# Performance work log

Measured on AMD Instinct MI355X. Metric: run time of the kernel, lower is better.

## Reference

```python
import jax, jax.numpy as jnp
import numpy as np
from jax import lax

B, H_IMG, W_IMG = 512, 812, 40
HID = 128
NUM_CLASSES = 12
LSTM_IN = 32 * ((W_IMG - 5) // 2 + 1)  # 32 channels * 18 = 576


def setup_inputs() -> dict:
    key = jax.random.key(0)
    ks = jax.random.split(key, 20)
    s = 0.05
    inp = {
        "x": jax.random.normal(ks[0], (B, 1, H_IMG, W_IMG), jnp.float32),
        "conv_w": jax.random.normal(ks[1], (32, 1, 20, 5), jnp.float32) * s,
        "conv_b": jax.random.normal(ks[2], (32,), jnp.float32) * s,
        "Wih0": jax.random.normal(ks[3], (4 * HID, LSTM_IN), jnp.float32) * s,
        "Whh0": jax.random.normal(ks[4], (4 * HID, HID), jnp.float32) * s,
        "bih0": jax.random.normal(ks[5], (4 * HID,), jnp.float32) * s,
        "bhh0": jax.random.normal(ks[6], (4 * HID,), jnp.float32) * s,
        "Wih1": jax.random.normal(ks[7], (4 * HID, HID), jnp.float32) * s,
        "Whh1": jax.random.normal(ks[8], (4 * HID, HID), jnp.float32) * s,
        "bih1": jax.random.normal(ks[9], (4 * HID,), jnp.float32) * s,
        "bhh1": jax.random.normal(ks[10], (4 * HID,), jnp.float32) * s,
        "W_att": jax.random.normal(ks[11], (HID, HID), jnp.float32) * s,
        "b_att": jax.random.normal(ks[12], (HID,), jnp.float32) * s,
        "v_att": jax.random.normal(ks[13], (HID,), jnp.float32) * s,
        "W1": jax.random.normal(ks[14], (64, HID), jnp.float32) * s,
        "b1": jax.random.normal(ks[15], (64,), jnp.float32) * s,
        "W2": jax.random.normal(ks[16], (NUM_CLASSES, 64), jnp.float32) * s,
        "b2": jax.random.normal(ks[17], (NUM_CLASSES,), jnp.float32) * s,
    }
    return inp


def _lstm_layer(seq, Wih, Whh, bih, bhh):
    # seq: (T, B, I); PyTorch gate order i, f, g, o
    T, Bn, _ = seq.shape
    Hd = Whh.shape[1]
    x_proj = jnp.einsum('tbi,gi->tbg', seq, Wih) + bih + bhh  # (T,B,4H)

    def step(carry, xg):
        h, c = carry
        g = xg + h @ Whh.T
        i, f, gg, o = jnp.split(g, 4, axis=-1)
        c = jax.nn.sigmoid(f) * c + jax.nn.sigmoid(i) * jnp.tanh(gg)
        h = jax.nn.sigmoid(o) * jnp.tanh(c)
        return (h, c), h

    init = (jnp.zeros((Bn, Hd), seq.dtype), jnp.zeros((Bn, Hd), seq.dtype))
    _, hs = lax.scan(step, init, x_proj)
    return hs  # (T,B,H)


def _forward(x, conv_w, conv_b, Wih0, Whh0, bih0, bhh0, Wih1, Whh1, bih1, bhh1,
             W_att, b_att, v_att, W1, b1, W2, b2):
    # Conv2d(1->32, k=(20,5), s=(8,2)) + ReLU
    y = lax.conv_general_dilated(x, conv_w, (8, 2), 'VALID',
                                 dimension_numbers=('NCHW', 'OIHW', 'NCHW'))
    y = jax.nn.relu(y + conv_b[None, :, None, None])  # (B,32,T,W')
    b, c, t, w = y.shape
    # permute(0,2,3,1).view(b,t,-1).permute(1,0,2) -> (T,B,W'*32)
    seq = jnp.transpose(y, (2, 0, 3, 1)).reshape(t, b, w * c)
    # 2-layer LSTM (inter-layer dropout=0.2 inactive at eval)
    h1 = _lstm_layer(seq, Wih0, Whh0, bih0, bhh0)
    h2 = _lstm_layer(h1, Wih1, Whh1, bih1, bhh1)
    # additive attention pooling over time
    squish = jnp.tanh(jnp.einsum('tbh,hk->tbk', h2, W_att) + b_att)  # (T,B,H)
    attn = jnp.einsum('tbh,h->tb', squish, v_att)                     # (T,B)
    w_att_n = jax.nn.softmax(attn, axis=0)                            # softmax over T
    pooled = jnp.einsum('tb,tbh->bh', w_att_n, h2)                    # (B,H)
    # dnn1 -> (dropout inactive at eval) -> output
    hdn = pooled @ W1.T + b1
    return hdn @ W2.T + b2  # (B,num_classes)


def reference(x, conv_w, conv_b, Wih0, Whh0, bih0, bhh0, Wih1, Whh1, bih1, bhh1,
              W_att, b_att, v_att, W1, b1, W2, b2):
    return _forward(x, conv_w, conv_b, Wih0, Whh0, bih0, bhh0, Wih1, Whh1,
                    bih1, bhh1, W_att, b_att, v_att, W1, b1, W2, b2)
```

## Files before the change

### kernel.cpp

```cpp
#include <hip/hip_runtime.h>
#include <stdint.h>


#define T_STEPS 100
#define BATCH   512
#define HIDD    128
#define GATES   512
#define LSTMIN  576
#define HIMG    812
#define WIMG    40

typedef __attribute__((ext_vector_type(8))) short bf16x8;
typedef __attribute__((ext_vector_type(4))) float f32x4;

__device__ inline unsigned short f2bf(float f) {
  unsigned u = __float_as_uint(f);
  unsigned r = (u + 0x7fffu + ((u >> 16) & 1u)) >> 16;
  return (unsigned short)r;
}
__device__ inline float bf2f(unsigned short b) {
  return __uint_as_float(((unsigned)b) << 16);
}
__device__ inline float fsigm(float x) {
  float e = __expf(-x);
  return __builtin_amdgcn_rcpf(1.f + e);
}
__device__ inline float ftanh(float x) {
  float e = __expf(2.f * x);
  return (e - 1.f) * __builtin_amdgcn_rcpf(e + 1.f);
}
__device__ inline void lds_barrier() {
  asm volatile("s_waitcnt lgkmcnt(0)" ::: "memory");
  __builtin_amdgcn_s_barrier();
}

__global__ void prep_kernel(const float* __restrict__ Wih0, const float* __restrict__ Whh0,
                            const float* __restrict__ Wih1, const float* __restrict__ Whh1,
                            const float* __restrict__ Watt, const float* __restrict__ convw,
                            const float* __restrict__ bih0, const float* __restrict__ bhh0,
                            const float* __restrict__ bih1, const float* __restrict__ bhh1,
                            unsigned short* __restrict__ wih0b, unsigned short* __restrict__ whh0b,
                            unsigned short* __restrict__ wih1b, unsigned short* __restrict__ whh1b,
                            unsigned short* __restrict__ wattb, float* __restrict__ convwt,
                            float* __restrict__ bias0, float* __restrict__ bias1) {
  int tid = blockIdx.x * blockDim.x + threadIdx.x;
  int stride = gridDim.x * blockDim.x;
  for (int i = tid; i < GATES * LSTMIN; i += stride) wih0b[i] = f2bf(Wih0[i]);
  for (int i = tid; i < GATES * HIDD; i += stride) whh0b[i] = f2bf(Whh0[i]);
  for (int i = tid; i < GATES * HIDD; i += stride) wih1b[i] = f2bf(Wih1[i]);
  for (int i = tid; i < GATES * HIDD; i += stride) whh1b[i] = f2bf(Whh1[i]);
  for (int i = tid; i < HIDD * HIDD; i += stride) {
    int j = i >> 7, k = i & 127;
    wattb[i] = f2bf(Watt[k * HIDD + j]);
  }
  for (int i = tid; i < 3200; i += stride) {
    int k = i >> 5, c = i & 31;
    convwt[i] = convw[c * 100 + k];
  }
  for (int i = tid; i < GATES; i += stride) bias0[i] = bih0[i] + bhh0[i];
  for (int i = tid; i < GATES; i += stride) bias1[i] = bih1[i] + bhh1[i];
}

__global__ __launch_bounds__(256) void conv_kernel(const float* __restrict__ x,
                                                   const float* __restrict__ convwt,
                                                   const float* __restrict__ convb,
                                                   unsigned short* __restrict__ seq) {
  __shared__ __align__(16) float img[212 * WIMG];
  const int b = blockIdx.x;
  const int chunk = blockIdx.y;
  const int t0 = chunk * 25;
  const int row0 = 8 * t0;
  const float4* src = (const float4*)(x + (size_t)b * (HIMG * WIMG) + (size_t)row0 * WIMG);
  float4* dst = (float4*)img;
  for (int i = threadIdx.x; i < 212 * WIMG / 4; i += 256) dst[i] = src[i];
  __syncthreads();
  for (int p = threadIdx.x; p < 450; p += 256) {
    int tl = p / 18, wp = p % 18;
    int t = t0 + tl;
    float acc[32];
#pragma unroll
    for (int c = 0; c < 32; ++c) acc[c] = 0.f;
    const float* ibase = img + (8 * tl) * WIMG + 2 * wp;
#pragma unroll 2
    for (int kh = 0; kh < 20; ++kh) {
#pragma unroll
      for (int kw = 0; kw < 5; ++kw) {
        float iv = ibase[kh * WIMG + kw];
        const float* wk = convwt + (kh * 5 + kw) * 32;
#pragma unroll
        for (int c = 0; c < 32; ++c) acc[c] = fmaf(iv, wk[c], acc[c]);
      }
    }
    unsigned short* o = seq + ((size_t)(t * BATCH + b)) * LSTMIN + wp * 32;
#pragma unroll
    for (int c = 0; c < 32; ++c) {
      float v = acc[c] + convb[c];
      o[c] = f2bf(v > 0.f ? v : 0.f);
    }
  }
}

template <int KDIM>
__global__ __launch_bounds__(256) void gemm_xp_kernel(const unsigned short* __restrict__ A,
                                                      const unsigned short* __restrict__ Bw,
                                                      const float* __restrict__ bias,
                                                      unsigned short* __restrict__ Xp) {
  __shared__ __align__(16) unsigned short As[128 * 32];
  __shared__ __align__(16) unsigned short Bs[128 * 32];
  const int tid = threadIdx.x;
  const int lane = tid & 63;
  const int w = tid >> 6;
  const int col16 = lane & 15;
  const int q = lane >> 4;
  const int n0 = blockIdx.x * 128;
  const int m0 = blockIdx.y * 128;
  const int wm = (w & 1) * 64;
  const int wn = (w >> 1) * 64;
  f32x4 acc[4][4] = {};
  const int r = tid >> 2;
  const int sw = ((tid & 3) ^ (r & 3)) * 8;
  const unsigned wslot = (unsigned)w * 512;
  const unsigned short* ga = A + (size_t)(m0 + r) * KDIM + sw;
  const unsigned short* gb = Bw + (size_t)(n0 + r) * KDIM + sw;
  for (int k0 = 0; k0 < KDIM; k0 += 32) {
    __syncthreads();
    __builtin_amdgcn_global_load_lds((const __attribute__((address_space(1))) void*)(ga + k0),
                                     (__attribute__((address_space(3))) void*)(As + wslot), 16, 0, 0);
    __builtin_amdgcn_global_load_lds((const __attribute__((address_space(1))) void*)(ga + k0 + (size_t)64 * KDIM),
                                     (__attribute__((address_space(3))) void*)(As + wslot + 2048), 16, 0, 0);
    __builtin_amdgcn_global_load_lds((const __attribute__((address_space(1))) void*)(gb + k0),
                                     (__attribute__((address_space(3))) void*)(Bs + wslot), 16, 0, 0);
    __builtin_amdgcn_global_load_lds((const __attribute__((address_space(1))) void*)(gb + k0 + (size_t)64 * KDIM),
                                     (__attribute__((address_space(3))) void*)(Bs + wslot + 2048), 16, 0, 0);
    __syncthreads();
    bf16x8 af[4], bv[4];
#pragma unroll
    for (int i = 0; i < 4; ++i) {
      int ra = wm + i * 16 + col16;
      af[i] = *(const bf16x8*)(As + ra * 32 + ((q ^ (ra & 3)) * 8));
      int rb2 = wn + i * 16 + col16;
      bv[i] = *(const bf16x8*)(Bs + rb2 * 32 + ((q ^ (rb2 & 3)) * 8));
    }
#pragma unroll
    for (int i = 0; i < 4; ++i)
#pragma unroll
      for (int j = 0; j < 4; ++j)
        acc[i][j] = __builtin_amdgcn_mfma_f32_16x16x32_bf16(af[i], bv[j], acc[i][j], 0, 0, 0);
  }
#pragma unroll
  for (int ct = 0; ct < 4; ++ct) {
    int n = n0 + wn + ct * 16 + col16;
    float bvv = bias[n];
    int wS = (n >> 4) & 7;
    int ntS = n >> 7;
    int c16S = n & 15;
#pragma unroll
    for (int rt = 0; rt < 4; ++rt) {
      int m = m0 + wm + rt * 16 + q * 4;
      int t = m >> 9;
      int bb = m & 511;
      int blk = bb >> 4;
      int r16 = bb & 15;
      ushort4 u;
      u.x = f2bf(acc[rt][ct][0] + bvv);
      u.y = f2bf(acc[rt][ct][1] + bvv);
      u.z = f2bf(acc[rt][ct][2] + bvv);
      u.w = f2bf(acc[rt][ct][3] + bvv);
      size_t tile = (((size_t)t * 32 + blk) * 8 + wS) * 4 + ntS;
      *(ushort4*)(Xp + tile * 256 + c16S * 16 + r16) = u;
    }
  }
}

__global__ __launch_bounds__(512, 2) void scan_kernel(const unsigned short* __restrict__ Xp,
                                                      const unsigned short* __restrict__ Whh,
                                                      unsigned short* __restrict__ hout) {
  __shared__ __align__(16) unsigned short hlds[16 * 136];
  const int tid = threadIdx.x;
  const int lane = tid & 63;
  const int w = tid >> 6;
  const int col16 = lane & 15;
  const int q = lane >> 4;
  const int rb = blockIdx.x * 16;
  const int blk = blockIdx.x;

  bf16x8 bfrag[4][4];
  const unsigned short* xpb[4];
#pragma unroll
  for (int nt = 0; nt < 4; ++nt) {
    int cn = nt * HIDD + w * 16 + col16;
#pragma unroll
    for (int ks = 0; ks < 4; ++ks)
      bfrag[nt][ks] = *(const bf16x8*)(Whh + (size_t)cn * HIDD + ks * 32 + q * 8);
    xpb[nt] = Xp + (((size_t)blk * 8 + w) * 4 + nt) * 256 + col16 * 16 + q * 4;
  }
  for (int i = tid; i < 16 * 136; i += 512) hlds[i] = 0;
  float cst[4] = {0.f, 0.f, 0.f, 0.f};
  uint2 xb[4][4];
#pragma unroll
  for (int nt = 0; nt < 4; ++nt) xb[0][nt] = *(const uint2*)(xpb[nt]);
#pragma unroll
  for (int nt = 0; nt < 4; ++nt) xb[1][nt] = *(const uint2*)(xpb[nt] + GATES * BATCH);
  __syncthreads();

  const int srow = tid >> 5;
  const int scol = (tid & 31) * 4;

#pragma unroll 4
  for (int t = 0; t < T_STEPS; ++t) {
    if (t + 2 < T_STEPS) {
      int s2 = (t + 2) & 3;
#pragma unroll
      for (int nt = 0; nt < 4; ++nt)
        xb[s2][nt] = *(const uint2*)(xpb[nt] + (size_t)(t + 2) * (GATES * BATCH));
    }
    bf16x8 af[4];
#pragma unroll
    for (int ks = 0; ks < 4; ++ks)
      af[ks] = *(const bf16x8*)(hlds + col16 * 136 + ks * 32 + q * 8);
    f32x4 acc[4];
    const int s = t & 3;
#pragma unroll
    for (int nt = 0; nt < 4; ++nt) {
      uint2 xv = xb[s][nt];
      acc[nt][0] = __uint_as_float(xv.x << 16);
      acc[nt][1] = __uint_as_float(xv.x & 0xffff0000u);
      acc[nt][2] = __uint_as_float(xv.y << 16);
      acc[nt][3] = __uint_as_float(xv.y & 0xffff0000u);
    }
#pragma unroll
    for (int ks = 0; ks < 4; ++ks)
#pragma unroll
      for (int nt = 0; nt < 4; ++nt)
        acc[nt] = __builtin_amdgcn_mfma_f32_16x16x32_bf16(af[ks], bfrag[nt][ks], acc[nt], 0, 0, 0);
    unsigned short hv[4];
#pragma unroll
    for (int rr = 0; rr < 4; ++rr) {
      float pi = acc[0][rr], pf = acc[1][rr];
      float pg = acc[2][rr], po = acc[3][rr];
      float cc = fsigm(pf) * cst[rr] + fsigm(pi) * ftanh(pg);
      cst[rr] = cc;
      hv[rr] = f2bf(fsigm(po) * ftanh(cc));
    }
    lds_barrier();
    {
      int hc = w * 16 + col16;
#pragma unroll
      for (int rr = 0; rr < 4; ++rr)
        hlds[(q * 4 + rr) * 136 + hc] = hv[rr];
    }
    lds_barrier();
    ushort4 hx = *(const ushort4*)(hlds + srow * 136 + scol);
    *(ushort4*)(hout + ((size_t)(t * BATCH) + rb + srow) * HIDD + scol) = hx;
  }
}

__global__ __launch_bounds__(256) void gemm_att_kernel(const unsigned short* __restrict__ A,
                                                       const unsigned short* __restrict__ Bw,
                                                       const float* __restrict__ b_att,
                                                       const float* __restrict__ v_att,
                                                       float* __restrict__ scores) {
  __shared__ __align__(16) unsigned short As[128 * 32];
  __shared__ __align__(16) unsigned short Bs[128 * 32];
  __shared__ float s_red[128];
  const int tid = threadIdx.x;
  const int lane = tid & 63;
  const int w = tid >> 6;
  const int col16 = lane & 15;
  const int q = lane >> 4;
  const int m0 = blockIdx.y * 128;
  const int wm = (w & 1) * 64;
  const int wn = (w >> 1) * 64;
  f32x4 acc[4][4] = {};
  const int r = tid >> 2;
  const int sw = ((tid & 3) ^ (r & 3)) * 8;
  const unsigned wslot = (unsigned)w * 512;
  const unsigned short* ga = A + (size_t)(m0 + r) * HIDD + sw;
  const unsigned short* gb = Bw + (size_t)r * HIDD + sw;
  for (int k0 = 0; k0 < HIDD; k0 += 32) {
    __syncthreads();
    __builtin_amdgcn_global_load_lds((const __attribute__((address_space(1))) void*)(ga + k0),
                                     (__attribute__((address_space(3))) void*)(As + wslot), 16, 0, 0);
    __builtin_amdgcn_global_load_lds((const __attribute__((address_space(1))) void*)(ga + k0 + (size_t)64 * HIDD),
                                     (__attribute__((address_space(3))) void*)(As + wslot + 2048), 16, 0, 0);
    __builtin_amdgcn_global_load_lds((const __attribute__((address_space(1))) void*)(gb + k0),
                                     (__attribute__((address_space(3))) void*)(Bs + wslot), 16, 0, 0);
    __builtin_amdgcn_global_load_lds((const __attribute__((address_space(1))) void*)(gb + k0 + (size_t)64 * HIDD),
                                     (__attribute__((address_space(3))) void*)(Bs + wslot + 2048), 16, 0, 0);
    __syncthreads();
    bf16x8 af[4], bv[4];
#pragma unroll
    for (int i = 0; i < 4; ++i) {
      int ra = wm + i * 16 + col16;
      af[i] = *(const bf16x8*)(As + ra * 32 + ((q ^ (ra & 3)) * 8));
      int rb2 = wn + i * 16 + col16;
      bv[i] = *(const bf16x8*)(Bs + rb2 * 32 + ((q ^ (rb2 & 3)) * 8));
    }
#pragma unroll
    for (int i = 0; i < 4; ++i)
#pragma unroll
      for (int j = 0; j < 4; ++j)
        acc[i][j] = __builtin_amdgcn_mfma_f32_16x16x32_bf16(af[i], bv[j], acc[i][j], 0, 0, 0);
  }
  if (tid < 128) s_red[tid] = 0.f;
  float rs[4][4];
#pragma unroll
  for (int rt = 0; rt < 4; ++rt)
#pragma unroll
    for (int rr = 0; rr < 4; ++rr) rs[rt][rr] = 0.f;
#pragma unroll
  for (int ct = 0; ct < 4; ++ct) {
    int n = wn + ct * 16 + col16;
    float bvv = b_att[n], vv = v_att[n];
#pragma unroll
    for (int rt = 0; rt < 4; ++rt)
#pragma unroll
      for (int rr = 0; rr < 4; ++rr) {
        float xv2 = acc[rt][ct][rr] + bvv;
        float e = __expf(2.f * xv2);
        rs[rt][rr] += vv * (e - 1.f) * __builtin_amdgcn_rcpf(e + 1.f);
      }
  }
#pragma unroll
  for (int off = 1; off < 16; off <<= 1)
#pragma unroll
    for (int rt = 0; rt < 4; ++rt)
#pragma unroll
      for (int rr = 0; rr < 4; ++rr) rs[rt][rr] += __shfl_xor(rs[rt][rr], off, 64);
  __syncthreads();
  if (col16 == 0) {
#pragma unroll
    for (int rt = 0; rt < 4; ++rt)
#pragma unroll
      for (int rr = 0; rr < 4; ++rr)
        atomicAdd(&s_red[wm + rt * 16 + q * 4 + rr], rs[rt][rr]);
  }
  __syncthreads();
  if (tid < 128) scores[m0 + tid] = s_red[tid];
}

__global__ __launch_bounds__(128) void final_kernel(const float* __restrict__ scores,
                                                    const unsigned short* __restrict__ h2,
                                                    const float* __restrict__ W1, const float* __restrict__ b1,
                                                    const float* __restrict__ W2, const float* __restrict__ b2,
                                                    float* __restrict__ out) {
  const int b = blockIdx.x;
  const int tid = threadIdx.x;
  __shared__ float wj[T_STEPS];
  __shared__ float red[128];
  __shared__ float pooled[128];
  __shared__ float hdn[64];
  float sv = (tid < T_STEPS) ? scores[tid * BATCH + b] : -1e30f;
  red[tid] = sv;
  __syncthreads();
#pragma unroll
  for (int off = 64; off > 0; off >>= 1) {
    if (tid < off) red[tid] = fmaxf(red[tid], red[tid + off]);
    __syncthreads();
  }
  float mx = red[0];
  __syncthreads();
  float ev = (tid < T_STEPS) ? __expf(sv - mx) : 0.f;
  red[tid] = ev;
  __syncthreads();
#pragma unroll
  for (int off = 64; off > 0; off >>= 1) {
    if (tid < off) red[tid] += red[tid + off];
    __syncthreads();
  }
  float inv = 1.0f / red[0];
  if (tid < T_STEPS) wj[tid] = ev * inv;
  __syncthreads();
  float p = 0.f;
  for (int t = 0; t < T_STEPS; ++t)
    p += wj[t] * bf2f(h2[((size_t)(t * BATCH + b)) * HIDD + tid]);
  pooled[tid] = p;
  __syncthreads();
  if (tid < 64) {
    float a = b1[tid];
    for (int h = 0; h < 128; ++h) a = fmaf(W1[tid * 128 + h], pooled[h], a);
    hdn[tid] = a;
  }
  __syncthreads();
  if (tid < 12) {
    float a = b2[tid];
    for (int j = 0; j < 64; ++j) a = fmaf(W2[tid * 64 + j], hdn[j], a);
    out[b * 12 + tid] = a;
  }
}

extern "C" void kernel_launch(void* const* d_in, const int* in_sizes, int n_in,
                              void* d_out, int out_size, void* d_ws, size_t ws_size,
                              hipStream_t stream) {
  (void)in_sizes; (void)n_in; (void)out_size; (void)ws_size;
  const float* x      = (const float*)d_in[0];
  const float* conv_w = (const float*)d_in[1];
  const float* conv_b = (const float*)d_in[2];
  const float* Wih0   = (const float*)d_in[3];
  const float* Whh0   = (const float*)d_in[4];
  const float* bih0   = (const float*)d_in[5];
  const float* bhh0   = (const float*)d_in[6];
  const float* Wih1   = (const float*)d_in[7];
  const float* Whh1   = (const float*)d_in[8];
  const float* bih1   = (const float*)d_in[9];
  const float* bhh1   = (const float*)d_in[10];
  const float* W_att  = (const float*)d_in[11];
  const float* b_att  = (const float*)d_in[12];
  const float* v_att  = (const float*)d_in[13];
  const float* W1     = (const float*)d_in[14];
  const float* b1     = (const float*)d_in[15];
  const float* W2     = (const float*)d_in[16];
  const float* b2     = (const float*)d_in[17];

  char* ws = (char*)d_ws;
  size_t off = 0;
  auto carve = [&](size_t bytes) { char* p = ws + off; off += (bytes + 255) & ~(size_t)255; return p; };
  unsigned short* seq    = (unsigned short*)carve((size_t)T_STEPS * BATCH * LSTMIN * 2);
  unsigned short* xp     = (unsigned short*)carve((size_t)T_STEPS * GATES * BATCH * 2);
  unsigned short* h1     = (unsigned short*)carve((size_t)T_STEPS * BATCH * HIDD * 2);
  unsigned short* h2     = (unsigned short*)carve((size_t)T_STEPS * BATCH * HIDD * 2);
  float*          scores = (float*)carve((size_t)T_STEPS * BATCH * 4);
  unsigned short* wih0b  = (unsigned short*)carve((size_t)GATES * LSTMIN * 2);
  unsigned short* whh0b  = (unsigned short*)carve((size_t)GATES * HIDD * 2);
  unsigned short* wih1b  = (unsigned short*)carve((size_t)GATES * HIDD * 2);
  unsigned short* whh1b  = (unsigned short*)carve((size_t)GATES * HIDD * 2);
  unsigned short* wattb  = (unsigned short*)carve((size_t)HIDD * HIDD * 2);
  float*          convwt = (float*)carve(3200 * 4);
  float*          bias0  = (float*)carve(GATES * 4);
  float*          bias1  = (float*)carve(GATES * 4);

  prep_kernel<<<256, 256, 0, stream>>>(Wih0, Whh0, Wih1, Whh1, W_att, conv_w,
                                       bih0, bhh0, bih1, bhh1,
                                       wih0b, whh0b, wih1b, whh1b, wattb, convwt, bias0, bias1);
  conv_kernel<<<dim3(512, 4), 256, 0, stream>>>(x, convwt, conv_b, seq);
  gemm_xp_kernel<LSTMIN><<<dim3(4, 400), 256, 0, stream>>>(seq, wih0b, bias0, xp);
  scan_kernel<<<32, 512, 0, stream>>>(xp, whh0b, h1);
  gemm_xp_kernel<HIDD><<<dim3(4, 400), 256, 0, stream>>>(h1, wih1b, bias1, xp);
  scan_kernel<<<32, 512, 0, stream>>>(xp, whh1b, h2);
  gemm_att_kernel<<<dim3(1, 400), 256, 0, stream>>>(h2, wattb, b_att, v_att, scores);
  final_kernel<<<512, 128, 0, stream>>>(scores, h2, W1, b1, W2, b2, (float*)d_out);
}
```

Before: 508.7 us.

## Fuse layer-1 input projection into layer-0 scan, use fp16 dot2 conv

The layer-0 scan now also multiplies each new hidden state by Wih1 with MFMA and writes the layer-1 gate pre-activations directly. This removes the h1 buffer and the second projection GEMM launch, at the cost of extra MFMA work and registers on the serial scan's critical path. The scan's h buffer is double-buffered so each step needs one barrier instead of two, and the h output store is deferred by one step. The convolution packs pairs of rows into fp16x2 and uses fdot2, halving FMA count but lowering input precision to fp16.

After: 500.8 us. Within noise of the previous version (-1.5%).

```diff
diff --git a/kernel.cpp b/kernel.cpp
--- a/kernel.cpp
+++ b/kernel.cpp
@@ -12,6 +12,7 @@
 
 typedef __attribute__((ext_vector_type(8))) short bf16x8;
 typedef __attribute__((ext_vector_type(4))) float f32x4;
+typedef __attribute__((ext_vector_type(2))) __fp16 f16x2;
 
 __device__ inline unsigned short f2bf(float f) {
   unsigned u = __float_as_uint(f);
@@ -41,7 +42,7 @@
                             const float* __restrict__ bih1, const float* __restrict__ bhh1,
                             unsigned short* __restrict__ wih0b, unsigned short* __restrict__ whh0b,
                             unsigned short* __restrict__ wih1b, unsigned short* __restrict__ whh1b,
-                            unsigned short* __restrict__ wattb, float* __restrict__ convwt,
+                            unsigned short* __restrict__ wattb, f16x2* __restrict__ wpair,
                             float* __restrict__ bias0, float* __restrict__ bias1) {
   int tid = blockIdx.x * blockDim.x + threadIdx.x;
   int stride = gridDim.x * blockDim.x;
@@ -53,26 +54,32 @@
     int j = i >> 7, k = i & 127;
     wattb[i] = f2bf(Watt[k * HIDD + j]);
   }
-  for (int i = tid; i < 3200; i += stride) {
-    int k = i >> 5, c = i & 31;
-    convwt[i] = convw[c * 100 + k];
+  for (int i = tid; i < 50 * 32; i += stride) {
+    int k2 = i >> 5, c = i & 31;
+    int kh2 = k2 / 5, kw = k2 % 5;
+    float lo = convw[c * 100 + (2 * kh2) * 5 + kw];
+    float hi = convw[c * 100 + (2 * kh2 + 1) * 5 + kw];
+    wpair[i] = __builtin_amdgcn_cvt_pkrtz(lo, hi);
   }
   for (int i = tid; i < GATES; i += stride) bias0[i] = bih0[i] + bhh0[i];
   for (int i = tid; i < GATES; i += stride) bias1[i] = bih1[i] + bhh1[i];
 }
 
 __global__ __launch_bounds__(256) void conv_kernel(const float* __restrict__ x,
-                                                   const float* __restrict__ convwt,
+                                                   const f16x2* __restrict__ wpair,
                                                    const float* __restrict__ convb,
                                                    unsigned short* __restrict__ seq) {
-  __shared__ __align__(16) float img[212 * WIMG];
+  __shared__ f16x2 imgp[106 * WIMG];
   const int b = blockIdx.x;
   const int chunk = blockIdx.y;
   const int t0 = chunk * 25;
-  const int row0 = 8 * t0;
-  const float4* src = (const float4*)(x + (size_t)b * (HIMG * WIMG) + (size_t)row0 * WIMG);
-  float4* dst = (float4*)img;
-  for (int i = threadIdx.x; i < 212 * WIMG / 4; i += 256) dst[i] = src[i];
+  const float* src = x + (size_t)b * (HIMG * WIMG) + (size_t)(8 * t0) * WIMG;
+  for (int i = threadIdx.x; i < 106 * WIMG; i += 256) {
+    int r2 = i / WIMG, c = i % WIMG;
+    float lo = src[(2 * r2) * WIMG + c];
+    float hi = src[(2 * r2 + 1) * WIMG + c];
+    imgp[i] = __builtin_amdgcn_cvt_pkrtz(lo, hi);
+  }
   __syncthreads();
   for (int p = threadIdx.x; p < 450; p += 256) {
     int tl = p / 18, wp = p % 18;
@@ -80,15 +87,16 @@
     float acc[32];
 #pragma unroll
     for (int c = 0; c < 32; ++c) acc[c] = 0.f;
-    const float* ibase = img + (8 * tl) * WIMG + 2 * wp;
+    const f16x2* ibase = imgp + (4 * tl) * WIMG + 2 * wp;
 #pragma unroll 2
-    for (int kh = 0; kh < 20; ++kh) {
+    for (int kh2 = 0; kh2 < 10; ++kh2) {
 #pragma unroll
       for (int kw = 0; kw < 5; ++kw) {
-        float iv = ibase[kh * WIMG + kw];
-        const float* wk = convwt + (kh * 5 + kw) * 32;
-#pragma unroll
-        for (int c = 0; c < 32; ++c) acc[c] = fmaf(iv, wk[c], acc[c]);
+        f16x2 iv = ibase[kh2 * WIMG + kw];
+        const f16x2* wk = wpair + (kh2 * 5 + kw) * 32;
+#pragma unroll
+        for (int c = 0; c < 32; ++c)
+          acc[c] = __builtin_amdgcn_fdot2(iv, wk[c], acc[c], false);
       }
     }
     unsigned short* o = seq + ((size_t)(t * BATCH + b)) * LSTMIN + wp * 32;
@@ -172,10 +180,14 @@
   }
 }
 
+template <bool FUSE_XP, bool WRITE_H>
 __global__ __launch_bounds__(512, 2) void scan_kernel(const unsigned short* __restrict__ Xp,
                                                       const unsigned short* __restrict__ Whh,
+                                                      const unsigned short* __restrict__ Wih_n,
+                                                      const float* __restrict__ bias_n,
+                                                      unsigned short* __restrict__ Xp_out,
                                                       unsigned short* __restrict__ hout) {
-  __shared__ __align__(16) unsigned short hlds[16 * 136];
+  __shared__ __align__(16) unsigned short hb[2][16 * 136];
   const int tid = threadIdx.x;
   const int lane = tid & 63;
   const int w = tid >> 6;
@@ -185,54 +197,82 @@
   const int blk = blockIdx.x;
 
   bf16x8 bfrag[4][4];
+  bf16x8 bfrag2[4][4];
   const unsigned short* xpb[4];
+  unsigned short* xob[4];
+  float biasn[4];
 #pragma unroll
   for (int nt = 0; nt < 4; ++nt) {
     int cn = nt * HIDD + w * 16 + col16;
 #pragma unroll
     for (int ks = 0; ks < 4; ++ks)
       bfrag[nt][ks] = *(const bf16x8*)(Whh + (size_t)cn * HIDD + ks * 32 + q * 8);
-    xpb[nt] = Xp + (((size_t)blk * 8 + w) * 4 + nt) * 256 + col16 * 16 + q * 4;
-  }
-  for (int i = tid; i < 16 * 136; i += 512) hlds[i] = 0;
+    if (FUSE_XP) {
+#pragma unroll
+      for (int ks = 0; ks < 4; ++ks)
+        bfrag2[nt][ks] = *(const bf16x8*)(Wih_n + (size_t)cn * HIDD + ks * 32 + q * 8);
+      biasn[nt] = bias_n[cn];
+    }
+    size_t tile = (((size_t)blk) * 8 + w) * 4 + nt;
+    xpb[nt] = Xp + tile * 256 + col16 * 16 + q * 4;
+    if (FUSE_XP) xob[nt] = Xp_out + tile * 256 + col16 * 16 + q * 4;
+  }
+  uint2 xb[2][4];
+#pragma unroll
+  for (int nt = 0; nt < 4; ++nt) xb[0][nt] = *(const uint2*)(xpb[nt]);
+#pragma unroll
+  for (int nt = 0; nt < 4; ++nt) xb[1][nt] = *(const uint2*)(xpb[nt] + GATES * BATCH);
+  for (int i = tid; i < 2 * 16 * 136; i += 512) hb[0][i] = 0;
   float cst[4] = {0.f, 0.f, 0.f, 0.f};
-  uint2 xb[4][4];
-#pragma unroll
-  for (int nt = 0; nt < 4; ++nt) xb[0][nt] = *(const uint2*)(xpb[nt]);
-#pragma unroll
-  for (int nt = 0; nt < 4; ++nt) xb[1][nt] = *(const uint2*)(xpb[nt] + GATES * BATCH);
-  __syncthreads();
+  lds_barrier();
 
   const int srow = tid >> 5;
   const int scol = (tid & 31) * 4;
-
-#pragma unroll 4
+  const int hc = w * 16 + col16;
+
+#pragma unroll 2
   for (int t = 0; t < T_STEPS; ++t) {
+    const int pb = (t & 1) ^ 1;
+    bf16x8 af[4];
+#pragma unroll
+    for (int ks = 0; ks < 4; ++ks)
+      af[ks] = *(const bf16x8*)(hb[pb] + col16 * 136 + ks * 32 + q * 8);
+    if (WRITE_H && t > 0) {
+      ushort4 hx = *(const ushort4*)(hb[pb] + srow * 136 + scol);
+      *(ushort4*)(hout + ((size_t)((t - 1) * BATCH) + rb + srow) * HIDD + scol) = hx;
+    }
+    const int s = t & 1;
+    uint2 xv[4];
+#pragma unroll
+    for (int nt = 0; nt < 4; ++nt) xv[nt] = xb[s][nt];
     if (t + 2 < T_STEPS) {
-      int s2 = (t + 2) & 3;
 #pragma unroll
       for (int nt = 0; nt < 4; ++nt)
-        xb[s2][nt] = *(const uint2*)(xpb[nt] + (size_t)(t + 2) * (GATES * BATCH));
-    }
-    bf16x8 af[4];
-#pragma unroll
-    for (int ks = 0; ks < 4; ++ks)
-      af[ks] = *(const bf16x8*)(hlds + col16 * 136 + ks * 32 + q * 8);
+        xb[s][nt] = *(const uint2*)(xpb[nt] + (size_t)(t + 2) * (GATES * BATCH));
+    }
     f32x4 acc[4];
-    const int s = t & 3;
 #pragma unroll
     for (int nt = 0; nt < 4; ++nt) {
-      uint2 xv = xb[s][nt];
-      acc[nt][0] = __uint_as_float(xv.x << 16);
-      acc[nt][1] = __uint_as_float(xv.x & 0xffff0000u);
-      acc[nt][2] = __uint_as_float(xv.y << 16);
-      acc[nt][3] = __uint_as_float(xv.y & 0xffff0000u);
+      acc[nt][0] = __uint_as_float(xv[nt].x << 16);
+      acc[nt][1] = __uint_as_float(xv[nt].x & 0xffff0000u);
+      acc[nt][2] = __uint_as_float(xv[nt].y << 16);
+      acc[nt][3] = __uint_as_float(xv[nt].y & 0xffff0000u);
     }
 #pragma unroll
     for (int ks = 0; ks < 4; ++ks)
 #pragma unroll
       for (int nt = 0; nt < 4; ++nt)
         acc[nt] = __builtin_amdgcn_mfma_f32_16x16x32_bf16(af[ks], bfrag[nt][ks], acc[nt], 0, 0, 0);
+    f32x4 acc2[4];
+    if (FUSE_XP) {
+#pragma unroll
+      for (int nt = 0; nt < 4; ++nt) acc2[nt] = f32x4{0.f, 0.f, 0.f, 0.f};
+#pragma unroll
+      for (int ks = 0; ks < 4; ++ks)
+#pragma unroll
+        for (int nt = 0; nt < 4; ++nt)
+          acc2[nt] = __builtin_amdgcn_mfma_f32_16x16x32_bf16(af[ks], bfrag2[nt][ks], acc2[nt], 0, 0, 0);
+    }
     unsigned short hv[4];
 #pragma unroll
     for (int rr = 0; rr < 4; ++rr) {
@@ -242,16 +282,50 @@
       cst[rr] = cc;
       hv[rr] = f2bf(fsigm(po) * ftanh(cc));
     }
+    if (FUSE_XP) {
+      if (t > 0) {
+#pragma unroll
+        for (int nt = 0; nt < 4; ++nt) {
+          ushort4 u;
+          u.x = f2bf(acc2[nt][0] + biasn[nt]);
+          u.y = f2bf(acc2[nt][1] + biasn[nt]);
+          u.z = f2bf(acc2[nt][2] + biasn[nt]);
+          u.w = f2bf(acc2[nt][3] + biasn[nt]);
+          *(ushort4*)(xob[nt] + (size_t)(t - 1) * (GATES * BATCH)) = u;
+        }
+      }
+    }
+#pragma unroll
+    for (int rr = 0; rr < 4; ++rr)
+      hb[t & 1][(q * 4 + rr) * 136 + hc] = hv[rr];
     lds_barrier();
-    {
-      int hc = w * 16 + col16;
-#pragma unroll
-      for (int rr = 0; rr < 4; ++rr)
-        hlds[(q * 4 + rr) * 136 + hc] = hv[rr];
-    }
-    lds_barrier();
-    ushort4 hx = *(const ushort4*)(hlds + srow * 136 + scol);
-    *(ushort4*)(hout + ((size_t)(t * BATCH) + rb + srow) * HIDD + scol) = hx;
+  }
+  if (WRITE_H) {
+    ushort4 hx = *(const ushort4*)(hb[(T_STEPS - 1) & 1] + srow * 136 + scol);
+    *(ushort4*)(hout + ((size_t)((T_STEPS - 1) * BATCH) + rb + srow) * HIDD + scol) = hx;
+  }
+  if (FUSE_XP) {
+    bf16x8 af[4];
+#pragma unroll
+    for (int ks = 0; ks < 4; ++ks)
+      af[ks] = *(const bf16x8*)(hb[(T_STEPS - 1) & 1] + col16 * 136 + ks * 32 + q * 8);
+    f32x4 acc2[4];
+#pragma unroll
+    for (int nt = 0; nt < 4; ++nt) acc2[nt] = f32x4{0.f, 0.f, 0.f, 0.f};
+#pragma unroll
+    for (int ks = 0; ks < 4; ++ks)
+#pragma unroll
+      for (int nt = 0; nt < 4; ++nt)
+        acc2[nt] = __builtin_amdgcn_mfma_f32_16x16x32_bf16(af[ks], bfrag2[nt][ks], acc2[nt], 0, 0, 0);
+#pragma unroll
+    for (int nt = 0; nt < 4; ++nt) {
+      ushort4 u;
+      u.x = f2bf(acc2[nt][0] + biasn[nt]);
+      u.y = f2bf(acc2[nt][1] + biasn[nt]);
+      u.z = f2bf(acc2[nt][2] + biasn[nt]);
+      u.w = f2bf(acc2[nt][3] + biasn[nt]);
+      *(ushort4*)(xob[nt] + (size_t)(T_STEPS - 1) * (GATES * BATCH)) = u;
+    }
   }
 }
 
@@ -416,8 +490,7 @@
   size_t off = 0;
   auto carve = [&](size_t bytes) { char* p = ws + off; off += (bytes + 255) & ~(size_t)255; return p; };
   unsigned short* seq    = (unsigned short*)carve((size_t)T_STEPS * BATCH * LSTMIN * 2);
-  unsigned short* xp     = (unsigned short*)carve((size_t)T_STEPS * GATES * BATCH * 2);
-  unsigned short* h1     = (unsigned short*)carve((size_t)T_STEPS * BATCH * HIDD * 2);
+  unsigned short* xp0    = (unsigned short*)carve((size_t)T_STEPS * GATES * BATCH * 2);
   unsigned short* h2     = (unsigned short*)carve((size_t)T_STEPS * BATCH * HIDD * 2);
   float*          scores = (float*)carve((size_t)T_STEPS * BATCH * 4);
   unsigned short* wih0b  = (unsigned short*)carve((size_t)GATES * LSTMIN * 2);
@@ -425,18 +498,18 @@
   unsigned short* wih1b  = (unsigned short*)carve((size_t)GATES * HIDD * 2);
   unsigned short* whh1b  = (unsigned short*)carve((size_t)GATES * HIDD * 2);
   unsigned short* wattb  = (unsigned short*)carve((size_t)HIDD * HIDD * 2);
-  float*          convwt = (float*)carve(3200 * 4);
+  f16x2*          wpair  = (f16x2*)carve(50 * 32 * 4);
   float*          bias0  = (float*)carve(GATES * 4);
   float*          bias1  = (float*)carve(GATES * 4);
+  unsigned short* xp1 = seq;
 
   prep_kernel<<<256, 256, 0, stream>>>(Wih0, Whh0, Wih1, Whh1, W_att, conv_w,
                                        bih0, bhh0, bih1, bhh1,
-                                       wih0b, whh0b, wih1b, whh1b, wattb, convwt, bias0, bias1);
-  conv_kernel<<<dim3(512, 4), 256, 0, stream>>>(x, convwt, conv_b, seq);
-  gemm_xp_kernel<LSTMIN><<<dim3(4, 400), 256, 0, stream>>>(seq, wih0b, bias0, xp);
-  scan_kernel<<<32, 512, 0, stream>>>(xp, whh0b, h1);
-  gemm_xp_kernel<HIDD><<<dim3(4, 400), 256, 0, stream>>>(h1, wih1b, bias1, xp);
-  scan_kernel<<<32, 512, 0, stream>>>(xp, whh1b, h2);
+                                       wih0b, whh0b, wih1b, whh1b, wattb, wpair, bias0, bias1);
+  conv_kernel<<<dim3(512, 4), 256, 0, stream>>>(x, wpair, conv_b, seq);
+  gemm_xp_kernel<LSTMIN><<<dim3(4, 400), 256, 0, stream>>>(seq, wih0b, bias0, xp0);
+  scan_kernel<true, false><<<32, 512, 0, stream>>>(xp0, whh0b, wih1b, bias1, xp1, nullptr);
+  scan_kernel<false, true><<<32, 512, 0, stream>>>(xp1, whh1b, nullptr, nullptr, nullptr, h2);
   gemm_att_kernel<<<dim3(1, 400), 256, 0, stream>>>(h2, wattb, b_att, v_att, scores);
   final_kernel<<<512, 128, 0, stream>>>(scores, h2, W1, b1, W2, b2, (float*)d_out);
 }
```
